# Kernel tuning notes

Hardware: AMD Instinct MI355X
Metric: run time of the kernel (lower is better)

The kernel has to match this reference:

```python
import jax, jax.numpy as jnp
import numpy as np

SQ2PI = 0.79788456
M, D_IN, H1, H2, D_OUT = 256, 784, 256, 256, 10


def setup_inputs() -> dict:
    key = jax.random.key(0)
    ks = jax.random.split(key, 6)
    x = jax.random.normal(ks[0], (M, D_IN), dtype=jnp.float32)
    target = jax.random.randint(ks[1], (M,), 0, D_OUT)

    def init_w(k, fan_in, fan_out):
        # torch init: uniform(-1/sqrt(size(1)), 1/sqrt(size(1))) * scale (scale=1)
        stdv = 1.0 / np.sqrt(fan_out)
        return jax.random.uniform(k, (fan_in, fan_out), jnp.float32, -stdv, stdv)

    w0 = init_w(ks[2], D_IN, H1)
    w1 = init_w(ks[3], H1, H2)
    w2 = init_w(ks[4], H2, H2)
    wlast = init_w(ks[5], H2, D_OUT)
    th0 = jnp.zeros((1, H1), jnp.float32)
    th1 = jnp.zeros((1, H2), jnp.float32)
    th2 = jnp.zeros((1, H2), jnp.float32)
    thlast = jnp.zeros((1, D_OUT), jnp.float32)
    return dict(x=x, target=target, w0=w0, w1=w1, w2=w2, wlast=wlast,
                th0=th0, th1=th1, th2=th2, thlast=thlast)


def _mvg_layer(xbar, xcov, m, th):
    # sigma[b] = m^T @ xcov[b] @ m + diag(sum_j 1 - m[j,:]^2)
    s = jnp.sum(1.0 - m ** 2, axis=0)                      # [H2]
    t = jnp.einsum('bjk,kl->bjl', xcov, m)                 # [B,H,H2]
    sigma = jnp.einsum('ji,bjl->bil', m, t) + jnp.diag(s)[None]  # [B,H2,H2]
    diagsig = jnp.diagonal(sigma, axis1=1, axis2=2)        # [B,H2]
    hbar = xbar @ m + th                                   # [B,H2]
    xbar_next = jnp.tanh(SQ2PI * hbar / jnp.sqrt(diagsig))
    c = (1.0 - xbar_next ** 2) / jnp.sqrt(diagsig)         # [B,H2]
    eye = jnp.eye(m.shape[1], dtype=xbar.dtype)
    xcov_next = (SQ2PI * sigma * c[:, :, None] * c[:, None, :]
                 + eye[None] * (1.0 - xbar_next[:, None, :] ** 2))
    return xbar_next, xcov_next


def reference(x, target, w0, w1, w2, wlast, th0, th1, th2, thlast):
    m0 = 2.0 * jax.nn.sigmoid(w0) - 1.0
    m1 = 2.0 * jax.nn.sigmoid(w1) - 1.0
    m2 = 2.0 * jax.nn.sigmoid(w2) - 1.0
    mlast = 2.0 * jax.nn.sigmoid(wlast) - 1.0

    # first layer: xcov for input is implicitly zero, sigma is diagonal
    diagsig1 = jnp.sum(1.0 - m0 ** 2, axis=0)              # [H1]
    h1bar = x @ m0 + th0                                   # [M,H1]
    x1bar = jnp.tanh(SQ2PI * h1bar / jnp.sqrt(diagsig1))
    eye1 = jnp.eye(m0.shape[1], dtype=x.dtype)
    xcov1 = eye1[None] * (1.0 - x1bar[:, None, :] ** 2)    # [M,H1,H1]

    x2bar, xcov2 = _mvg_layer(x1bar, xcov1, m1, th1)
    x3bar, xcov3 = _mvg_layer(x2bar, xcov2, m2, th2)

    hlastbar = x3bar @ mlast + thlast                      # [M,10]
    logprobs = jax.nn.log_softmax(hlastbar, axis=-1)
    loss = -jnp.mean(jnp.take_along_axis(logprobs, target[:, None], axis=1))
    pred = jnp.argmax(hlastbar, axis=1)
    frac_correct = jnp.mean((pred == target).astype(jnp.float32))
    return (hlastbar, logprobs, xcov3, loss, frac_correct)
```

## Files before the change

kernel.cpp:

```cpp
#include <hip/hip_runtime.h>
#include <math.h>

#define SQ2PI_F 0.79788456f

typedef __attribute__((ext_vector_type(8))) short short8;
typedef __attribute__((ext_vector_type(4))) float f32x4;
typedef __attribute__((ext_vector_type(4))) unsigned short u16x4;
typedef __attribute__((address_space(1))) unsigned int gas_u32;
typedef __attribute__((address_space(3))) unsigned int las_u32;

__device__ inline unsigned short bf16rne(float x) {
  unsigned int u = __float_as_uint(x);
  u += 0x7fffu + ((u >> 16) & 1u);
  return (unsigned short)(u >> 16);
}
__device__ inline float bf2f(unsigned short u) {
  return __uint_as_float(((unsigned int)u) << 16);
}

__global__ void k_prep(const float* __restrict__ w0, const float* __restrict__ w1,
                       const float* __restrict__ w2, const float* __restrict__ wlast,
                       float* __restrict__ m0, float* __restrict__ m1,
                       unsigned short* __restrict__ m1th, float* __restrict__ m2,
                       unsigned short* __restrict__ m2th, float* __restrict__ mlast,
                       float* __restrict__ lf) {
  int b = blockIdx.x, t = threadIdx.x;
  if (b < 784) {
    int i = b * 256 + t;
    m0[i] = tanhf(0.5f * w0[i]);
  } else if (b < 1040) {
    int j = b - 784;
    float v = tanhf(0.5f * w1[j * 256 + t]);
    m1[j * 256 + t] = v;
    m1th[t * 256 + j] = bf16rne(v);
  } else if (b < 1296) {
    int j = b - 1040;
    float v = tanhf(0.5f * w2[j * 256 + t]);
    m2[j * 256 + t] = v;
    m2th[t * 256 + j] = bf16rne(v);
  } else {
    int i = (b - 1296) * 256 + t;
    if (i < 2560) mlast[i] = tanhf(0.5f * wlast[i]);
    if (b == 1296 && t < 2) lf[t] = 0.f;
  }
}

__global__ void k_layer1(const float* __restrict__ x, const float* __restrict__ m0,
                         const float* __restrict__ th0,
                         float* __restrict__ x1bar, float* __restrict__ d1) {
  __shared__ float xr[784];
  __shared__ float ph[256], pd[256];
  int r = blockIdx.x, t = threadIdx.x;
  int j = t & 255, h = t >> 8;
  for (int p = t; p < 784; p += 512) xr[p] = x[r * 784 + p];
  __syncthreads();
  float acch = 0.f, accd = 0.f;
  int k0 = h * 392, k1 = k0 + 392;
#pragma unroll 8
  for (int k = k0; k < k1; ++k) {
    float mm = m0[k * 256 + j];
    acch = fmaf(xr[k], mm, acch);
    accd = fmaf(-mm, mm, accd + 1.f);
  }
  if (h) { ph[j] = acch; pd[j] = accd; }
  __syncthreads();
  if (!h) {
    acch += ph[j];
    accd += pd[j];
    float rs = rsqrtf(accd);
    float xb = tanhf(SQ2PI_F * (acch + th0[j]) * rs);
    x1bar[r * 256 + j] = xb;
    d1[r * 256 + j] = 1.f - xb * xb;
  }
}

__global__ void k_layer2(const float* __restrict__ d1, const float* __restrict__ x1bar,
                         const float* __restrict__ m1, const float* __restrict__ m2,
                         const float* __restrict__ th1, const float* __restrict__ th2,
                         float* __restrict__ c2, float* __restrict__ d2p,
                         float* __restrict__ h3bar,
                         float* __restrict__ s1g, float* __restrict__ s2g) {
  __shared__ float pd[256], ph[256], ps[256], sx[256], p3[256], q2[256];
  int r = blockIdx.x, t = threadIdx.x;
  int i = t & 255, h = t >> 8;
  int j0 = h * 128, j1 = j0 + 128;
  float accd = 0.f, acch = 0.f, accs = 0.f;
  for (int j = j0; j < j1; ++j) {
    float mm = m1[j * 256 + i];
    accd = fmaf(d1[r * 256 + j] * mm, mm, accd);
    acch = fmaf(x1bar[r * 256 + j], mm, acch);
    accs = fmaf(-mm, mm, accs + 1.f);
  }
  if (h) { pd[i] = accd; ph[i] = acch; ps[i] = accs; }
  __syncthreads();
  if (!h) {
    accd += pd[i];
    acch += ph[i];
    accs += ps[i];
    float rs = rsqrtf(accd + accs);
    float xb = tanhf(SQ2PI_F * (acch + th1[i]) * rs);
    float d = 1.f - xb * xb;
    c2[r * 256 + i] = d * rs;
    d2p[r * 256 + i] = d;
    sx[i] = xb;
    if (r == 0) s1g[i] = accs;
  }
  __syncthreads();
  float acc3 = 0.f, acc2 = 0.f;
  for (int j = j0; j < j1; ++j) {
    float mm = m2[j * 256 + i];
    acc3 = fmaf(sx[j], mm, acc3);
    acc2 = fmaf(-mm, mm, acc2 + 1.f);
  }
  if (h) { p3[i] = acc3; q2[i] = acc2; }
  __syncthreads();
  if (!h) {
    h3bar[r * 256 + i] = acc3 + p3[i] + th2[i];
    if (r == 0) s2g[i] = acc2 + q2[i];
  }
}

__global__ __launch_bounds__(512) void k_fused(
    const unsigned short* __restrict__ m1th, const unsigned short* __restrict__ m2th,
    const float* __restrict__ d1, const float* __restrict__ c2,
    const float* __restrict__ d2p, const float* __restrict__ s1,
    const float* __restrict__ s2, const float* __restrict__ h3bar,
    float* __restrict__ x3bar, float* __restrict__ xcov3) {
  __shared__ __align__(16) unsigned short SB[2][8192];
  __shared__ __align__(16) unsigned short XB[2][8192];
  __shared__ float c2L[256], d2pL[256], s1L[256], s2L[256];
  __shared__ float dsig[256], c3L[256], d3L[256];

  const int b = blockIdx.x;
  const int tid = threadIdx.x;
  const int l = tid & 63, w = tid >> 6;
  const int lr = l & 15, lk = l >> 4;
  const int R = w * 32;

  auto stage_panel = [&](const unsigned short* gsrc, unsigned short* sb) {
#pragma unroll
    for (int q = 0; q < 2; ++q) {
      int rl = q * 16 + w * 2 + (l >> 5);
      int ch = l & 31;
      const unsigned short* src = gsrc + rl * 256 + ((ch ^ (rl & 7)) << 3);
      unsigned short* dst = sb + (q * 16 + w * 2) * 256;
      __builtin_amdgcn_global_load_lds((const gas_u32*)src, (las_u32*)dst, 16, 0, 0);
    }
  };

#define PREAD(SBASE, p, kc)                                   \
  (*(const short8*)((const char*)(SBASE) + ((p) << 9) +      \
                    ((unsigned)((((kc) ^ ((p) & 7))) << 4))))

  stage_panel(m1th, SB[0]);

  if (tid < 256) {
    c2L[tid] = c2[b * 256 + tid];
    d2pL[tid] = d2p[b * 256 + tid];
    s1L[tid] = s1[tid];
    s2L[tid] = s2[tid];
  }

  const float* d1b = d1 + b * 256;

  short8 af_w[2][8];
#pragma unroll
  for (int ks = 0; ks < 8; ++ks) {
    f32x4 dv0 = *(const f32x4*)(d1b + ks * 32 + lk * 8);
    f32x4 dv1 = *(const f32x4*)(d1b + ks * 32 + lk * 8 + 4);
#pragma unroll
    for (int f = 0; f < 2; ++f) {
      short8 mv = *(const short8*)(m1th + (size_t)(R + f * 16 + lr) * 256 + ks * 32 + lk * 8);
#pragma unroll
      for (int e = 0; e < 4; ++e) {
        af_w[f][ks][e] = (short)bf16rne(bf2f((unsigned short)mv[e]) * dv0[e]);
        af_w[f][ks][e + 4] = (short)bf16rne(bf2f((unsigned short)mv[e + 4]) * dv1[e]);
      }
    }
  }
  __syncthreads();

  short8 afX[2][8];

#pragma unroll
  for (int cp = 0; cp < 8; ++cp) {
    if (cp < 7)
      stage_panel(m1th + (size_t)(cp + 1) * 32 * 256, SB[(cp + 1) & 1]);
    else
      stage_panel(m2th, SB[0]);
    const unsigned short* sbc = SB[cp & 1];
    f32x4 acc[2][2];
#pragma unroll
    for (int i = 0; i < 2; ++i)
#pragma unroll
      for (int j = 0; j < 2; ++j) acc[i][j] = {0.f, 0.f, 0.f, 0.f};
#pragma unroll
    for (int ks = 0; ks < 8; ++ks) {
      short8 bq[2];
#pragma unroll
      for (int f = 0; f < 2; ++f) bq[f] = PREAD(sbc, f * 16 + lr, ks * 4 + lk);
#pragma unroll
      for (int i = 0; i < 2; ++i)
#pragma unroll
        for (int j = 0; j < 2; ++j)
          acc[i][j] = __builtin_amdgcn_mfma_f32_16x16x32_bf16(af_w[i][ks], bq[j], acc[i][j], 0, 0, 0);
    }
    char* XP = (char*)XB[cp & 1];
#pragma unroll
    for (int i = 0; i < 2; ++i) {
      int r0 = R + i * 16 + lk * 4;
#pragma unroll
      for (int j = 0; j < 2; ++j) {
        int p = j * 16 + lr;
        int cc = cp * 32 + p;
        float c2c = c2L[cc];
        u16x4 st;
#pragma unroll
        for (int e = 0; e < 4; ++e) {
          int r = r0 + e;
          float g = acc[i][j][e];
          if (r == cc) g += s1L[r];
          float v = SQ2PI_F * c2L[r] * c2c * g;
          if (r == cc) v += d2pL[r];
          st[e] = bf16rne(v);
        }
        *(u16x4*)(XP + (p << 9) + (((unsigned)(r0 << 1)) ^ ((p & 7) << 4))) = st;
      }
    }
    __syncthreads();
    if (w == cp) {
#pragma unroll
      for (int f = 0; f < 2; ++f) {
        int p2 = f * 16 + lr;
#pragma unroll
        for (int ks = 0; ks < 8; ++ks)
          afX[f][ks] = PREAD(XP, p2, ks * 4 + lk);
      }
    }
  }

  short8 am2[2][8];
#pragma unroll
  for (int f = 0; f < 2; ++f)
#pragma unroll
    for (int ks = 0; ks < 8; ++ks)
      am2[f][ks] = *(const short8*)(m2th + (size_t)(R + f * 16 + lr) * 256 + ks * 32 + lk * 8);

  f32x4 sig[8][2][2];
#pragma unroll
  for (int lp = 0; lp < 8; ++lp)
#pragma unroll
    for (int i = 0; i < 2; ++i)
#pragma unroll
      for (int j = 0; j < 2; ++j) sig[lp][i][j] = {0.f, 0.f, 0.f, 0.f};

#define STAGE2(N) stage_panel(m2th + (size_t)(N) * 32 * 256, SB[(N) & 1]);

#define STEP1(LP)                                                                          \
  {                                                                                        \
    const unsigned short* sb1 = SB[(LP) & 1];                                              \
    char* TB = (char*)XB[(LP) & 1];                                                        \
    f32x4 at[2][2];                                                                        \
    _Pragma("unroll") for (int i = 0; i < 2; ++i) _Pragma("unroll")                        \
        for (int j = 0; j < 2; ++j) at[i][j] = {0.f, 0.f, 0.f, 0.f};                       \
    _Pragma("unroll") for (int ks = 0; ks < 8; ++ks) {                                     \
      short8 bq[2];                                                                        \
      _Pragma("unroll") for (int f = 0; f < 2; ++f)                                        \
          bq[f] = PREAD(sb1, f * 16 + lr, ks * 4 + lk);                                    \
      _Pragma("unroll") for (int i = 0; i < 2; ++i) _Pragma("unroll")                      \
          for (int j = 0; j < 2; ++j) at[i][j] =                                           \
              __builtin_amdgcn_mfma_f32_16x16x32_bf16(afX[i][ks], bq[j], at[i][j], 0, 0, 0); \
    }                                                                                      \
    _Pragma("unroll") for (int i = 0; i < 2; ++i) {                                        \
      int j0 = R + i * 16 + lk * 4;                                                        \
      _Pragma("unroll") for (int jf = 0; jf < 2; ++jf) {                                   \
        int p = jf * 16 + lr;                                                              \
        u16x4 st;                                                                          \
        _Pragma("unroll") for (int e = 0; e < 4; ++e) st[e] = bf16rne(at[i][jf][e]);       \
        *(u16x4*)(TB + (p << 9) + (((unsigned)(j0 << 1)) ^ ((p & 7) << 4))) = st;          \
      }                                                                                    \
    }                                                                                      \
  }

#define STEP2(LP)                                                                          \
  {                                                                                        \
    const char* TB = (const char*)XB[(LP) & 1];                                            \
    _Pragma("unroll") for (int ks = 0; ks < 8; ++ks) {                                     \
      short8 bq2[2];                                                                       \
      _Pragma("unroll") for (int f = 0; f < 2; ++f)                                        \
          bq2[f] = PREAD(TB, f * 16 + lr, ks * 4 + lk);                                    \
      _Pragma("unroll") for (int i = 0; i < 2; ++i) _Pragma("unroll")                      \
          for (int j = 0; j < 2; ++j) sig[LP][i][j] =                                      \
              __builtin_amdgcn_mfma_f32_16x16x32_bf16(am2[i][ks], bq2[j], sig[LP][i][j], 0, 0, 0); \
    }                                                                                      \
    if (w == (LP) && lk == (lr >> 2)) {                                                    \
      _Pragma("unroll") for (int lf = 0; lf < 2; ++lf) {                                   \
        f32x4 v4 = sig[LP][lf][lf];                                                        \
        dsig[R + lf * 16 + lr] = v4[lr & 3];                                               \
      }                                                                                    \
    }                                                                                      \
  }

  STAGE2(1) STEP1(0)
  __syncthreads();
  STAGE2(2) STEP1(1) STEP2(0)
  __syncthreads();
  STAGE2(3) STEP1(2) STEP2(1)
  __syncthreads();
  STAGE2(4) STEP1(3) STEP2(2)
  __syncthreads();
  STAGE2(5) STEP1(4) STEP2(3)
  __syncthreads();
  STAGE2(6) STEP1(5) STEP2(4)
  __syncthreads();
  STAGE2(7) STEP1(6) STEP2(5)
  __syncthreads();
  STEP1(7) STEP2(6)
  __syncthreads();
  STEP2(7)
  __syncthreads();
#undef STEP1
#undef STEP2
#undef STAGE2
#undef PREAD

  if (tid < 256) {
    float ds = dsig[tid] + s2L[tid];
    float rs = rsqrtf(ds);
    float xb = tanhf(SQ2PI_F * h3bar[b * 256 + tid] * rs);
    x3bar[b * 256 + tid] = xb;
    float d = 1.f - xb * xb;
    c3L[tid] = d * rs;
    d3L[tid] = d;
  }
  __syncthreads();

#pragma unroll
  for (int lp = 0; lp < 8; ++lp) {
#pragma unroll
    for (int ifg = 0; ifg < 2; ++ifg) {
      int i0 = R + ifg * 16 + lk * 4;
#pragma unroll
      for (int lf = 0; lf < 2; ++lf) {
        int gl = lp * 32 + lf * 16 + lr;
        float cg = c3L[gl];
        f32x4 st;
#pragma unroll
        for (int e = 0; e < 4; ++e) {
          int i = i0 + e;
          float g = sig[lp][ifg][lf][e];
          if (i == gl) g += s2L[i];
          float v = SQ2PI_F * c3L[i] * cg * g;
          if (i == gl) v += d3L[i];
          st[e] = v;
        }
        *(f32x4*)(xcov3 + ((size_t)b << 16) + (size_t)gl * 256 + i0) = st;
      }
    }
  }
}

__global__ void k_final4(const float* __restrict__ x3bar, const float* __restrict__ mlast,
                         const float* __restrict__ thlast, const int* __restrict__ target,
                         float* __restrict__ hlast_out, float* __restrict__ logp_out,
                         float* __restrict__ loss_out, float* __restrict__ frac_out) {
  __shared__ float Wl[2560];
  int t = threadIdx.x;
  int r = blockIdx.x * 64 + t;
  for (int p = t; p < 2560; p += 64) Wl[p] = mlast[p];
  __syncthreads();
  float acc[10];
#pragma unroll
  for (int c = 0; c < 10; ++c) acc[c] = thlast[c];
  for (int j = 0; j < 256; ++j) {
    float xv = x3bar[r * 256 + j];
#pragma unroll
    for (int c = 0; c < 10; ++c) acc[c] = fmaf(xv, Wl[j * 10 + c], acc[c]);
  }
#pragma unroll
  for (int c = 0; c < 10; ++c) hlast_out[r * 10 + c] = acc[c];
  float mx = acc[0];
  int am = 0;
#pragma unroll
  for (int c = 1; c < 10; ++c)
    if (acc[c] > mx) { mx = acc[c]; am = c; }
  float se = 0.f;
#pragma unroll
  for (int c = 0; c < 10; ++c) se += expf(acc[c] - mx);
  float lse = logf(se);
#pragma unroll
  for (int c = 0; c < 10; ++c) logp_out[r * 10 + c] = acc[c] - mx - lse;
  int tg = target[r];
  float lossc = -(acc[tg] - mx - lse) * (1.f / 256.f);
  float corr = (am == tg) ? (1.f / 256.f) : 0.f;
#pragma unroll
  for (int off = 32; off > 0; off >>= 1) {
    lossc += __shfl_down(lossc, off);
    corr += __shfl_down(corr, off);
  }
  if (t == 0) {
    atomicAdd(loss_out, lossc);
    atomicAdd(frac_out, corr);
  }
}


extern "C" void kernel_launch(void* const* d_in, const int* in_sizes, int n_in,
                              void* d_out, int out_size, void* d_ws, size_t ws_size,
                              hipStream_t stream) {
  const float* x = (const float*)d_in[0];
  const int* target = (const int*)d_in[1];
  const float* w0 = (const float*)d_in[2];
  const float* w1 = (const float*)d_in[3];
  const float* w2 = (const float*)d_in[4];
  const float* wlast = (const float*)d_in[5];
  const float* th0 = (const float*)d_in[6];
  const float* th1 = (const float*)d_in[7];
  const float* th2 = (const float*)d_in[8];
  const float* thlast = (const float*)d_in[9];

  float* W = (float*)d_ws;
  size_t o = 0;
  auto alloc = [&](size_t n) { float* p = W + o; o += n; return p; };
  float* m0 = alloc(200704);
  float* m1 = alloc(65536);
  float* m2 = alloc(65536);
  float* mlast = alloc(2560);
  float* s1 = alloc(256);
  float* s2 = alloc(256);
  float* x1bar = alloc(65536);
  float* d1 = alloc(65536);
  float* c2 = alloc(65536);
  float* d2p = alloc(65536);
  float* h3bar = alloc(65536);
  float* x3bar = alloc(65536);
  unsigned short* m1th = (unsigned short*)alloc(32768);
  unsigned short* m2th = (unsigned short*)alloc(32768);

  float* hlast = (float*)d_out;
  float* logp = hlast + 2560;
  float* xcov3_out = logp + 2560;
  float* loss = xcov3_out + 16777216;
  float* frac = loss + 1;

  k_prep<<<1306, 256, 0, stream>>>(w0, w1, w2, wlast, m0, m1, m1th, m2, m2th,
                                   mlast, loss);
  k_layer1<<<256, 512, 0, stream>>>(x, m0, th0, x1bar, d1);
  k_layer2<<<256, 512, 0, stream>>>(d1, x1bar, m1, m2, th1, th2, c2, d2p,
                                    h3bar, s1, s2);
  k_fused<<<256, 512, 0, stream>>>(m1th, m2th, d1, c2, d2p, s1, s2,
                                   h3bar, x3bar, xcov3_out);
  k_final4<<<4, 64, 0, stream>>>(x3bar, mlast, thlast, target, hlast, logp, loss, frac);
}
```

Baseline: 131.2 us.

## Restructure fused layer-3 covariance to 1024 threads with fp8 second GEMM

Doubles the fused kernel's block to 1024 threads, each wave owning 16 rows instead of 32. The intermediate product xcov2·m2 is stored in LDS as fp8 for the whole 256x256 tile instead of streaming through double buffers. The diagonal of sigma is computed by a separate dot-product pass, and the final m2ᵀ·T GEMM uses fp8 MFMA with a precomputed fp8 copy of m2. This aims to cut MFMA and register cost and to simplify the staged pipeline. It risks accuracy loss from fp8 e4m3 on the covariance intermediates, and 64KB+ of LDS allows only one block per CU.

```diff
diff --git a/kernel.cpp b/kernel.cpp
--- a/kernel.cpp
+++ b/kernel.cpp
@@ -1,4 +1,5 @@
 #include <hip/hip_runtime.h>
+#include <hip/hip_fp8.h>
 #include <math.h>
 
 #define SQ2PI_F 0.79788456f
@@ -17,13 +18,23 @@
 __device__ inline float bf2f(unsigned short u) {
   return __uint_as_float(((unsigned int)u) << 16);
 }
+__device__ inline unsigned int pk_fp8x4(f32x4 v) {
+  __hip_fp8_e4m3 a(v[0]), b(v[1]), c(v[2]), d(v[3]);
+  return (unsigned int)a.__x | ((unsigned int)b.__x << 8) |
+         ((unsigned int)c.__x << 16) | ((unsigned int)d.__x << 24);
+}
+__device__ inline float fp8tof(unsigned char b) {
+  __hip_fp8_e4m3 h;
+  h.__x = (__hip_fp8_storage_t)b;
+  return (float)h;
+}
 
 __global__ void k_prep(const float* __restrict__ w0, const float* __restrict__ w1,
                        const float* __restrict__ w2, const float* __restrict__ wlast,
                        float* __restrict__ m0, float* __restrict__ m1,
                        unsigned short* __restrict__ m1th, float* __restrict__ m2,
-                       unsigned short* __restrict__ m2th, float* __restrict__ mlast,
-                       float* __restrict__ lf) {
+                       unsigned short* __restrict__ m2th, unsigned char* __restrict__ m2f8,
+                       float* __restrict__ mlast, float* __restrict__ lf) {
   int b = blockIdx.x, t = threadIdx.x;
   if (b < 784) {
     int i = b * 256 + t;
@@ -38,6 +49,7 @@
     float v = tanhf(0.5f * w2[j * 256 + t]);
     m2[j * 256 + t] = v;
     m2th[t * 256 + j] = bf16rne(v);
+    m2f8[t * 256 + j] = __hip_fp8_e4m3(v).__x;
   } else {
     int i = (b - 1296) * 256 + t;
     if (i < 2560) mlast[i] = tanhf(0.5f * wlast[i]);
@@ -120,32 +132,31 @@
   }
 }
 
-__global__ __launch_bounds__(512) void k_fused(
+__global__ __launch_bounds__(1024) void k_fused(
     const unsigned short* __restrict__ m1th, const unsigned short* __restrict__ m2th,
-    const float* __restrict__ d1, const float* __restrict__ c2,
-    const float* __restrict__ d2p, const float* __restrict__ s1,
-    const float* __restrict__ s2, const float* __restrict__ h3bar,
-    float* __restrict__ x3bar, float* __restrict__ xcov3) {
+    const unsigned char* __restrict__ m2f8, const float* __restrict__ d1,
+    const float* __restrict__ c2, const float* __restrict__ d2p,
+    const float* __restrict__ s1, const float* __restrict__ s2,
+    const float* __restrict__ h3bar, float* __restrict__ x3bar,
+    float* __restrict__ xcov3) {
+  __shared__ __align__(16) unsigned char XC[65536];
   __shared__ __align__(16) unsigned short SB[2][8192];
-  __shared__ __align__(16) unsigned short XB[2][8192];
   __shared__ float c2L[256], d2pL[256], s1L[256], s2L[256];
-  __shared__ float dsig[256], c3L[256], d3L[256];
+  __shared__ float c3L[256], d3L[256];
+  __shared__ float pq[1024];
 
   const int b = blockIdx.x;
   const int tid = threadIdx.x;
   const int l = tid & 63, w = tid >> 6;
   const int lr = l & 15, lk = l >> 4;
-  const int R = w * 32;
+  const int R = w * 16;
 
   auto stage_panel = [&](const unsigned short* gsrc, unsigned short* sb) {
-#pragma unroll
-    for (int q = 0; q < 2; ++q) {
-      int rl = q * 16 + w * 2 + (l >> 5);
-      int ch = l & 31;
-      const unsigned short* src = gsrc + rl * 256 + ((ch ^ (rl & 7)) << 3);
-      unsigned short* dst = sb + (q * 16 + w * 2) * 256;
-      __builtin_amdgcn_global_load_lds((const gas_u32*)src, (las_u32*)dst, 16, 0, 0);
-    }
+    int rl = w * 2 + (l >> 5);
+    int ch = l & 31;
+    const unsigned short* src = gsrc + rl * 256 + ((ch ^ (rl & 7)) << 3);
+    unsigned short* dst = sb + (w * 2) * 256;
+    __builtin_amdgcn_global_load_lds((const gas_u32*)src, (las_u32*)dst, 16, 0, 0);
   };
 
 #define PREAD(SBASE, p, kc)                                   \
@@ -163,169 +174,109 @@
 
   const float* d1b = d1 + b * 256;
 
-  short8 af_w[2][8];
+  short8 af_w[8];
 #pragma unroll
   for (int ks = 0; ks < 8; ++ks) {
     f32x4 dv0 = *(const f32x4*)(d1b + ks * 32 + lk * 8);
     f32x4 dv1 = *(const f32x4*)(d1b + ks * 32 + lk * 8 + 4);
-#pragma unroll
-    for (int f = 0; f < 2; ++f) {
-      short8 mv = *(const short8*)(m1th + (size_t)(R + f * 16 + lr) * 256 + ks * 32 + lk * 8);
-#pragma unroll
-      for (int e = 0; e < 4; ++e) {
-        af_w[f][ks][e] = (short)bf16rne(bf2f((unsigned short)mv[e]) * dv0[e]);
-        af_w[f][ks][e + 4] = (short)bf16rne(bf2f((unsigned short)mv[e + 4]) * dv1[e]);
-      }
-    }
-  }
-  __syncthreads();
-
-  short8 afX[2][8];
+    short8 mv = *(const short8*)(m1th + (size_t)(R + lr) * 256 + ks * 32 + lk * 8);
+#pragma unroll
+    for (int e = 0; e < 4; ++e) {
+      af_w[ks][e] = (short)bf16rne(bf2f((unsigned short)mv[e]) * dv0[e]);
+      af_w[ks][e + 4] = (short)bf16rne(bf2f((unsigned short)mv[e + 4]) * dv1[e]);
+    }
+  }
+  __syncthreads();
+
+  short8 afX[8];
+  unsigned short(*XB)[8192] = (unsigned short(*)[8192])XC;
 
 #pragma unroll
   for (int cp = 0; cp < 8; ++cp) {
     if (cp < 7)
-      stage_panel(m1th + (size_t)(cp + 1) * 32 * 256, SB[(cp + 1) & 1]);
+      stage_panel(m1th + (size_t)(cp + 1) * 8192, SB[(cp + 1) & 1]);
     else
       stage_panel(m2th, SB[0]);
     const unsigned short* sbc = SB[cp & 1];
-    f32x4 acc[2][2];
-#pragma unroll
-    for (int i = 0; i < 2; ++i)
-#pragma unroll
-      for (int j = 0; j < 2; ++j) acc[i][j] = {0.f, 0.f, 0.f, 0.f};
+    f32x4 acc[2];
+    acc[0] = {0.f, 0.f, 0.f, 0.f};
+    acc[1] = {0.f, 0.f, 0.f, 0.f};
 #pragma unroll
     for (int ks = 0; ks < 8; ++ks) {
-      short8 bq[2];
-#pragma unroll
-      for (int f = 0; f < 2; ++f) bq[f] = PREAD(sbc, f * 16 + lr, ks * 4 + lk);
-#pragma unroll
-      for (int i = 0; i < 2; ++i)
-#pragma unroll
-        for (int j = 0; j < 2; ++j)
-          acc[i][j] = __builtin_amdgcn_mfma_f32_16x16x32_bf16(af_w[i][ks], bq[j], acc[i][j], 0, 0, 0);
+      short8 bq0 = PREAD(sbc, lr, ks * 4 + lk);
+      short8 bq1 = PREAD(sbc, 16 + lr, ks * 4 + lk);
+      acc[0] = __builtin_amdgcn_mfma_f32_16x16x32_bf16(af_w[ks], bq0, acc[0], 0, 0, 0);
+      acc[1] = __builtin_amdgcn_mfma_f32_16x16x32_bf16(af_w[ks], bq1, acc[1], 0, 0, 0);
     }
     char* XP = (char*)XB[cp & 1];
-#pragma unroll
-    for (int i = 0; i < 2; ++i) {
-      int r0 = R + i * 16 + lk * 4;
-#pragma unroll
-      for (int j = 0; j < 2; ++j) {
-        int p = j * 16 + lr;
-        int cc = cp * 32 + p;
-        float c2c = c2L[cc];
-        u16x4 st;
-#pragma unroll
-        for (int e = 0; e < 4; ++e) {
-          int r = r0 + e;
-          float g = acc[i][j][e];
-          if (r == cc) g += s1L[r];
-          float v = SQ2PI_F * c2L[r] * c2c * g;
-          if (r == cc) v += d2pL[r];
-          st[e] = bf16rne(v);
-        }
-        *(u16x4*)(XP + (p << 9) + (((unsigned)(r0 << 1)) ^ ((p & 7) << 4))) = st;
+    int r0 = R + lk * 4;
+#pragma unroll
+    for (int j = 0; j < 2; ++j) {
+      int p = j * 16 + lr;
+      int cc = cp * 32 + p;
+      float c2c = c2L[cc];
+      u16x4 st;
+#pragma unroll
+      for (int e = 0; e < 4; ++e) {
+        int r = r0 + e;
+        float g = acc[j][e];
+        if (r == cc) g += s1L[r];
+        float v = SQ2PI_F * c2L[r] * c2c * g;
+        if (r == cc) v += d2pL[r];
+        st[e] = bf16rne(v);
       }
+      *(u16x4*)(XP + (p << 9) + (((unsigned)(r0 << 1)) ^ ((p & 7) << 4))) = st;
     }
     __syncthreads();
-    if (w == cp) {
-#pragma unroll
-      for (int f = 0; f < 2; ++f) {
-        int p2 = f * 16 + lr;
-#pragma unroll
-        for (int ks = 0; ks < 8; ++ks)
-          afX[f][ks] = PREAD(XP, p2, ks * 4 + lk);
-      }
-    }
-  }
-
-  short8 am2[2][8];
-#pragma unroll
-  for (int f = 0; f < 2; ++f)
-#pragma unroll
-    for (int ks = 0; ks < 8; ++ks)
-      am2[f][ks] = *(const short8*)(m2th + (size_t)(R + f * 16 + lr) * 256 + ks * 32 + lk * 8);
-
-  f32x4 sig[8][2][2];
-#pragma unroll
-  for (int lp = 0; lp < 8; ++lp)
-#pragma unroll
-    for (int i = 0; i < 2; ++i)
-#pragma unroll
-      for (int j = 0; j < 2; ++j) sig[lp][i][j] = {0.f, 0.f, 0.f, 0.f};
-
-#define STAGE2(N) stage_panel(m2th + (size_t)(N) * 32 * 256, SB[(N) & 1]);
-
-#define STEP1(LP)                                                                          \
-  {                                                                                        \
-    const unsigned short* sb1 = SB[(LP) & 1];                                              \
-    char* TB = (char*)XB[(LP) & 1];                                                        \
-    f32x4 at[2][2];                                                                        \
-    _Pragma("unroll") for (int i = 0; i < 2; ++i) _Pragma("unroll")                        \
-        for (int j = 0; j < 2; ++j) at[i][j] = {0.f, 0.f, 0.f, 0.f};                       \
-    _Pragma("unroll") for (int ks = 0; ks < 8; ++ks) {                                     \
-      short8 bq[2];                                                                        \
-      _Pragma("unroll") for (int f = 0; f < 2; ++f)                                        \
-          bq[f] = PREAD(sb1, f * 16 + lr, ks * 4 + lk);                                    \
-      _Pragma("unroll") for (int i = 0; i < 2; ++i) _Pragma("unroll")                      \
-          for (int j = 0; j < 2; ++j) at[i][j] =                                           \
-              __builtin_amdgcn_mfma_f32_16x16x32_bf16(afX[i][ks], bq[j], at[i][j], 0, 0, 0); \
-    }                                                                                      \
-    _Pragma("unroll") for (int i = 0; i < 2; ++i) {                                        \
-      int j0 = R + i * 16 + lk * 4;                                                        \
-      _Pragma("unroll") for (int jf = 0; jf < 2; ++jf) {                                   \
-        int p = jf * 16 + lr;                                                              \
-        u16x4 st;                                                                          \
-        _Pragma("unroll") for (int e = 0; e < 4; ++e) st[e] = bf16rne(at[i][jf][e]);       \
-        *(u16x4*)(TB + (p << 9) + (((unsigned)(j0 << 1)) ^ ((p & 7) << 4))) = st;          \
-      }                                                                                    \
-    }                                                                                      \
-  }
-
-#define STEP2(LP)                                                                          \
-  {                                                                                        \
-    const char* TB = (const char*)XB[(LP) & 1];                                            \
-    _Pragma("unroll") for (int ks = 0; ks < 8; ++ks) {                                     \
-      short8 bq2[2];                                                                       \
-      _Pragma("unroll") for (int f = 0; f < 2; ++f)                                        \
-          bq2[f] = PREAD(TB, f * 16 + lr, ks * 4 + lk);                                    \
-      _Pragma("unroll") for (int i = 0; i < 2; ++i) _Pragma("unroll")                      \
-          for (int j = 0; j < 2; ++j) sig[LP][i][j] =                                      \
-              __builtin_amdgcn_mfma_f32_16x16x32_bf16(am2[i][ks], bq2[j], sig[LP][i][j], 0, 0, 0); \
-    }                                                                                      \
-    if (w == (LP) && lk == (lr >> 2)) {                                                    \
-      _Pragma("unroll") for (int lf = 0; lf < 2; ++lf) {                                   \
-        f32x4 v4 = sig[LP][lf][lf];                                                        \
-        dsig[R + lf * 16 + lr] = v4[lr & 3];                                               \
-      }                                                                                    \
-    }                                                                                      \
-  }
-
-  STAGE2(1) STEP1(0)
-  __syncthreads();
-  STAGE2(2) STEP1(1) STEP2(0)
-  __syncthreads();
-  STAGE2(3) STEP1(2) STEP2(1)
-  __syncthreads();
-  STAGE2(4) STEP1(3) STEP2(2)
-  __syncthreads();
-  STAGE2(5) STEP1(4) STEP2(3)
-  __syncthreads();
-  STAGE2(6) STEP1(5) STEP2(4)
-  __syncthreads();
-  STAGE2(7) STEP1(6) STEP2(5)
-  __syncthreads();
-  STEP1(7) STEP2(6)
-  __syncthreads();
-  STEP2(7)
-  __syncthreads();
-#undef STEP1
-#undef STEP2
-#undef STAGE2
-#undef PREAD
+    if (cp == (w >> 1)) {
+      int p2 = (w & 1) * 16 + lr;
+#pragma unroll
+      for (int ks = 0; ks < 8; ++ks) afX[ks] = PREAD(XP, p2, ks * 4 + lk);
+    }
+  }
+
+#pragma unroll
+  for (int lp = 0; lp < 8; ++lp) {
+    if (lp < 7) stage_panel(m2th + (size_t)(lp + 1) * 8192, SB[(lp + 1) & 1]);
+    const unsigned short* sbt = SB[lp & 1];
+    f32x4 at[2];
+    at[0] = {0.f, 0.f, 0.f, 0.f};
+    at[1] = {0.f, 0.f, 0.f, 0.f};
+#pragma unroll
+    for (int ks = 0; ks < 8; ++ks) {
+      short8 bq0 = PREAD(sbt, lr, ks * 4 + lk);
+      short8 bq1 = PREAD(sbt, 16 + lr, ks * 4 + lk);
+      at[0] = __builtin_amdgcn_mfma_f32_16x16x32_bf16(afX[ks], bq0, at[0], 0, 0, 0);
+      at[1] = __builtin_amdgcn_mfma_f32_16x16x32_bf16(afX[ks], bq1, at[1], 0, 0, 0);
+    }
+    int j0 = R + lk * 4;
+#pragma unroll
+    for (int jf = 0; jf < 2; ++jf) {
+      int lq = lp * 32 + jf * 16 + lr;
+      unsigned int pk = pk_fp8x4(at[jf]);
+      *(unsigned int*)(XC + (lq << 8) + ((((j0 >> 3) ^ (lq & 7)) << 3) + (j0 & 7))) = pk;
+    }
+    __syncthreads();
+  }
+
+  {
+    int lq = tid >> 2, q = tid & 3;
+    float s = 0.f;
+#pragma unroll
+    for (int jc = q * 8; jc < q * 8 + 8; ++jc) {
+      unsigned long long c8 =
+          *(const unsigned long long*)(XC + (lq << 8) + ((jc ^ (lq & 7)) << 3));
+      short8 mv = *(const short8*)(m2th + (size_t)lq * 256 + jc * 8);
+#pragma unroll
+      for (int e = 0; e < 8; ++e)
+        s = fmaf(bf2f((unsigned short)mv[e]), fp8tof((unsigned char)(c8 >> (8 * e))), s);
+    }
+    pq[tid] = s;
+  }
+  __syncthreads();
 
   if (tid < 256) {
-    float ds = dsig[tid] + s2L[tid];
+    float ds = pq[tid * 4] + pq[tid * 4 + 1] + pq[tid * 4 + 2] + pq[tid * 4 + 3] + s2L[tid];
     float rs = rsqrtf(ds);
     float xb = tanhf(SQ2PI_F * h3bar[b * 256 + tid] * rs);
     x3bar[b * 256 + tid] = xb;
@@ -335,29 +286,43 @@
   }
   __syncthreads();
 
+  long am2[8];
+#pragma unroll
+  for (int ks = 0; ks < 8; ++ks)
+    am2[ks] = *(const long*)(m2f8 + (size_t)(R + lr) * 256 + ks * 32 + lk * 8);
+
 #pragma unroll
   for (int lp = 0; lp < 8; ++lp) {
-#pragma unroll
-    for (int ifg = 0; ifg < 2; ++ifg) {
-      int i0 = R + ifg * 16 + lk * 4;
-#pragma unroll
-      for (int lf = 0; lf < 2; ++lf) {
-        int gl = lp * 32 + lf * 16 + lr;
-        float cg = c3L[gl];
-        f32x4 st;
-#pragma unroll
-        for (int e = 0; e < 4; ++e) {
-          int i = i0 + e;
-          float g = sig[lp][ifg][lf][e];
-          if (i == gl) g += s2L[i];
-          float v = SQ2PI_F * c3L[i] * cg * g;
-          if (i == gl) v += d3L[i];
-          st[e] = v;
-        }
-        *(f32x4*)(xcov3 + ((size_t)b << 16) + (size_t)gl * 256 + i0) = st;
+    f32x4 sc[2];
+    sc[0] = {0.f, 0.f, 0.f, 0.f};
+    sc[1] = {0.f, 0.f, 0.f, 0.f};
+    int p0 = lp * 32 + lr, p1 = lp * 32 + 16 + lr;
+#pragma unroll
+    for (int ks = 0; ks < 8; ++ks) {
+      long bq0 = *(const long*)(XC + (p0 << 8) + (((ks * 4 + lk) ^ (p0 & 7)) << 3));
+      long bq1 = *(const long*)(XC + (p1 << 8) + (((ks * 4 + lk) ^ (p1 & 7)) << 3));
+      sc[0] = __builtin_amdgcn_mfma_f32_16x16x32_fp8_fp8(am2[ks], bq0, sc[0], 0, 0, 0);
+      sc[1] = __builtin_amdgcn_mfma_f32_16x16x32_fp8_fp8(am2[ks], bq1, sc[1], 0, 0, 0);
+    }
+    int i0 = R + lk * 4;
+#pragma unroll
+    for (int lf = 0; lf < 2; ++lf) {
+      int gl = lp * 32 + lf * 16 + lr;
+      float cg = c3L[gl];
+      f32x4 st;
+#pragma unroll
+      for (int e = 0; e < 4; ++e) {
+        int i = i0 + e;
+        float g = sc[lf][e];
+        if (i == gl) g += s2L[i];
+        float v = SQ2PI_F * c3L[i] * cg * g;
+        if (i == gl) v += d3L[i];
+        st[e] = v;
       }
-    }
-  }
+      *(f32x4*)(xcov3 + ((size_t)b << 16) + (size_t)gl * 256 + i0) = st;
+    }
+  }
+#undef PREAD
 }
 
 __global__ void k_final4(const float* __restrict__ x3bar, const float* __restrict__ mlast,
@@ -436,6 +401,7 @@
   float* x3bar = alloc(65536);
   unsigned short* m1th = (unsigned short*)alloc(32768);
   unsigned short* m2th = (unsigned short*)alloc(32768);
+  unsigned char* m2f8 = (unsigned char*)alloc(16384);
 
   float* hlast = (float*)d_out;
   float* logp = hlast + 2560;
@@ -444,11 +410,11 @@
   float* frac = loss + 1;
 
   k_prep<<<1306, 256, 0, stream>>>(w0, w1, w2, wlast, m0, m1, m1th, m2, m2th,
-                                   mlast, loss);
+                                   m2f8, mlast, loss);
   k_layer1<<<256, 512, 0, stream>>>(x, m0, th0, x1bar, d1);
   k_layer2<<<256, 512, 0, stream>>>(d1, x1bar, m1, m2, th1, th2, c2, d2p,
                                     h3bar, s1, s2);
-  k_fused<<<256, 512, 0, stream>>>(m1th, m2th, d1, c2, d2p, s1, s2,
-                                   h3bar, x3bar, xcov3_out);
+  k_fused<<<256, 1024, 0, stream>>>(m1th, m2th, m2f8, d1, c2, d2p, s1, s2,
+                                    h3bar, x3bar, xcov3_out);
   k_final4<<<4, 64, 0, stream>>>(x3bar, mlast, thlast, target, hlast, logp, loss, frac);
 }
```

Result: slower. 138.8 us (+5.8%).
